# Kernel tuning notes

Hardware: AMD Instinct MI355X
Metric: run time of the kernel (lower is better)

The kernel has to match this reference:

```python
import jax, jax.numpy as jnp
import numpy as np

N, E, IN, HID, OUT = 50000, 800000, 128, 96, 2


def setup_inputs() -> dict:
    key = jax.random.key(0)
    ks = jax.random.split(key, 10)
    x = jax.random.normal(ks[0], (N, IN), jnp.float32)
    edge_index = jax.random.randint(ks[1], (2, E), 0, N, dtype=jnp.int64)
    # PQVA mask: per-node, first output channel is a "known" quantity (masked out),
    # second is the prediction target -> ~mask selects exactly N elements.
    m = np.zeros((N, OUT), dtype=bool)
    m[:, 0] = True
    PQVA_mask = jnp.asarray(m)
    scaler_mean = 0.1 * jax.random.normal(ks[2], (IN,), jnp.float32)
    scaler_std = 0.5 + jax.random.uniform(ks[3], (IN,), jnp.float32)  # in [0.5, 1.5)
    W1 = jax.random.normal(ks[4], (IN, HID), jnp.float32) / np.sqrt(IN)
    W2 = jax.random.normal(ks[5], (HID, HID), jnp.float32) / np.sqrt(HID)
    W3 = jax.random.normal(ks[6], (HID, HID), jnp.float32) / np.sqrt(HID)
    Wout = jax.random.normal(ks[7], (HID, OUT), jnp.float32) / np.sqrt(HID)
    b1 = jnp.zeros((HID,), jnp.float32)
    b2 = jnp.zeros((HID,), jnp.float32)
    b3 = jnp.zeros((HID,), jnp.float32)
    bout = jnp.zeros((OUT,), jnp.float32)
    return {"x": x, "edge_index": edge_index, "PQVA_mask": PQVA_mask,
            "scaler_mean": scaler_mean, "scaler_std": scaler_std,
            "W1": W1, "b1": b1, "W2": W2, "b2": b2, "W3": W3, "b3": b3,
            "Wout": Wout, "bout": bout}


def reference(x, edge_index, PQVA_mask, scaler_mean, scaler_std,
              W1, b1, W2, b2, W3, b3, Wout, bout):
    n = x.shape[0]
    loop = jnp.arange(n, dtype=edge_index.dtype)
    src = jnp.concatenate([edge_index[0], loop])  # add self-loops (GCNConv default)
    dst = jnp.concatenate([edge_index[1], loop])
    deg = jax.ops.segment_sum(jnp.ones_like(dst, x.dtype), dst, num_segments=n)
    dinv = jax.lax.rsqrt(deg)  # deg >= 1 thanks to self-loops
    norm = (dinv[src] * dinv[dst])[:, None]  # [E+N, 1]

    def prop(h):  # D^-1/2 (A+I) D^-1/2 @ h  via gather-scale-scatter
        return jax.ops.segment_sum(h[src] * norm, dst, num_segments=n)

    h = (x - scaler_mean) / scaler_std          # standard scaler
    h = jax.nn.relu(prop(h @ W1) + b1)          # GCNConv 1 + ReLU
    h = jax.nn.relu(prop(h @ W2) + b2)          # GCNConv 2 + ReLU
    h = prop(h @ W3) + b3                       # GCNConv 3 (last, no act)
    out = h @ Wout + bout                       # final Linear -> [N, OUT]
    # masked reshape: ~mask has exactly one True per node -> [N]
    return out.reshape(-1)[~PQVA_mask.reshape(-1)]
```

## Files before the change

### kernel.cpp

```cpp
#include <hip/hip_runtime.h>
#include <hip/hip_fp16.h>

#define IN_F 128
#define HID_F 96
#define PB 512
#define STRIDE 6144
#define MAXB 8192

typedef _Float16 f16x8 __attribute__((ext_vector_type(8)));
typedef float f32x4 __attribute__((ext_vector_type(4)));

__device__ __forceinline__ void swizzle_one(const float* W, __half* Wsw, int idx) {
    int j  = idx & 7;
    int ln = (idx >> 3) & 63;
    int ct = idx >> 9;
    int t = ct % 6, c = ct / 6;
    int k   = c * 32 + (ln >> 4) * 8 + j;
    int col = t * 16 + (ln & 15);
    Wsw[idx] = (__half)W[k * 96 + col];
}


__global__ __launch_bounds__(256) void part_prep_kernel(
        const int* __restrict__ srcv, const int* __restrict__ dstv,
        int* __restrict__ bcur, int* __restrict__ ebuf, int E,
        const float* __restrict__ stdv, float* __restrict__ rstd,
        const float* __restrict__ W3, const float* __restrict__ Wout,
        const float* __restrict__ b3, const float* __restrict__ bout,
        float* __restrict__ wv, float* __restrict__ cconst,
        const float* __restrict__ W1, __half* __restrict__ Wsw1, int SW1,
        const float* __restrict__ W2, __half* __restrict__ Wsw2, int SW2) {
    int b = blockIdx.x, t = threadIdx.x;
    if (b >= PB) {
        int pb = b - PB;
        if (pb == 0) {
            if (t < IN_F) rstd[t] = 1.0f / stdv[t];
            if (t < HID_F) {
                float s = 0.f;
                for (int j = 0; j < HID_F; ++j) s += W3[t * HID_F + j] * Wout[j * 2 + 1];
                wv[t] = s;
            }
            if (t == 0) {
                float s = 0.f;
                for (int j = 0; j < HID_F; ++j) s += b3[j] * Wout[j * 2 + 1];
                cconst[0] = s + bout[1];
            }
        } else if (pb <= 48) {
            int idx = (pb - 1) * 256 + t;
            if (idx < SW1) swizzle_one(W1, Wsw1, idx);
        } else {
            int idx = (pb - 49) * 256 + t;
            if (idx < SW2) swizzle_one(W2, Wsw2, idx);
        }
        return;
    }
    __shared__ int h[256];
    __shared__ int cur[256];
    int chunk = (E + PB - 1) / PB;
    int s = b * chunk;
    int eend = min(s + chunk, E);
    h[t] = 0;
    __syncthreads();
    for (int e = s + t; e < eend; e += 256) atomicAdd(&h[dstv[e] >> 8], 1);
    __syncthreads();
    if (h[t]) cur[t] = t * STRIDE + atomicAdd(&bcur[t], h[t]);
    __syncthreads();
    for (int e = s + t; e < eend; e += 256) {
        int sv = srcv[e], d = dstv[e];
        int p = atomicAdd(&cur[d >> 8], 1);
        ebuf[p] = (sv << 8) | (d & 255);
    }
}


__global__ __launch_bounds__(256) void buildcsr_kernel(
        const int* __restrict__ ebuf, const int* __restrict__ bcur,
        int* __restrict__ rowdeg, float* __restrict__ dinv,
        int* __restrict__ cols, int n) {
    __shared__ int dg[256];
    __shared__ int tmp[256];
    __shared__ int cur[256];
    __shared__ int colst[MAXB];
    int t = threadIdx.x;
    int k = blockIdx.x;
    int seg = k * STRIDE;
    int cnt = min(bcur[k], STRIDE);
    dg[t] = 0;
    __syncthreads();
    for (int i = t; i < cnt; i += 256) atomicAdd(&dg[ebuf[seg + i] & 255], 1);
    __syncthreads();
    int v = dg[t];
    tmp[t] = v;
    __syncthreads();
#pragma unroll
    for (int off = 1; off < 256; off <<= 1) {
        int u = (t >= off) ? tmp[t - off] : 0;
        __syncthreads();
        tmp[t] += u;
        __syncthreads();
    }
    int excl = tmp[t] - v;
    int node = (k << 8) + t;
    if (node < n) {
        rowdeg[node] = ((seg + excl) << 9) | v;
        dinv[node] = rsqrtf((float)v + 1.0f);
    }
    cur[t] = excl;
    __syncthreads();
    for (int i = t; i < cnt; i += 256) {
        int p = ebuf[seg + i];
        int lp = atomicAdd(&cur[p & 255], 1);
        colst[lp] = ((unsigned)p) >> 8;
    }
    __syncthreads();
    for (int i = t; i < cnt; i += 256) cols[seg + i] = colst[i];
}


template<int MODE, int K>
__global__ __launch_bounds__(256) void gemm_mfma_kernel(
        const void* __restrict__ Ain, const __half* __restrict__ Wsw,
        const float* __restrict__ mean, const float* __restrict__ rstd,
        const float* __restrict__ dinv, __half* __restrict__ C, int n) {
    constexpr int NCH = K / 32;
    int lane = threadIdx.x & 63;
    int wv_  = threadIdx.x >> 6;
    int m = lane & 15, q = lane >> 4;
    int node0 = blockIdx.x * 64 + wv_ * 16;
    int g = node0 + m;
    int gc = g < n ? g : n - 1;

    f32x4 acc[6];
#pragma unroll
    for (int t = 0; t < 6; ++t) acc[t] = (f32x4){0.f, 0.f, 0.f, 0.f};

#pragma unroll
    for (int c = 0; c < NCH; ++c) {
        f16x8 a;
        if (MODE == 0) {
            const float* ap = (const float*)Ain + (long)gc * K + c * 32 + q * 8;
            float4 v0 = *(const float4*)ap;
            float4 v1 = *(const float4*)(ap + 4);
            float4 m0 = *(const float4*)(mean + c * 32 + q * 8);
            float4 m1 = *(const float4*)(mean + c * 32 + q * 8 + 4);
            float4 r0 = *(const float4*)(rstd + c * 32 + q * 8);
            float4 r1 = *(const float4*)(rstd + c * 32 + q * 8 + 4);
            a[0] = (_Float16)((v0.x - m0.x) * r0.x);
            a[1] = (_Float16)((v0.y - m0.y) * r0.y);
            a[2] = (_Float16)((v0.z - m0.z) * r0.z);
            a[3] = (_Float16)((v0.w - m0.w) * r0.w);
            a[4] = (_Float16)((v1.x - m1.x) * r1.x);
            a[5] = (_Float16)((v1.y - m1.y) * r1.y);
            a[6] = (_Float16)((v1.z - m1.z) * r1.z);
            a[7] = (_Float16)((v1.w - m1.w) * r1.w);
        } else {
            a = *(const f16x8*)((const __half*)Ain + (long)gc * K + c * 32 + q * 8);
        }
#pragma unroll
        for (int t = 0; t < 6; ++t) {
            f16x8 b = *(const f16x8*)(Wsw + (size_t)(((c * 6) + t) * 64 + lane) * 8);
            acc[t] = __builtin_amdgcn_mfma_f32_16x16x32_f16(a, b, acc[t], 0, 0, 0);
        }
    }
    float dv[4];
#pragma unroll
    for (int r = 0; r < 4; ++r) {
        int gr = node0 + q * 4 + r;
        dv[r] = (gr < n) ? dinv[gr] : 0.f;
    }
#pragma unroll
    for (int t = 0; t < 6; ++t)
#pragma unroll
        for (int r = 0; r < 4; ++r) {
            int gr = node0 + q * 4 + r;
            if (gr < n) C[(long)gr * 96 + t * 16 + m] = (__half)(acc[t][r] * dv[r]);
        }
}


template<int DOT>
__global__ __launch_bounds__(256) void prop16_kernel(
        const __half* __restrict__ hin, const int* __restrict__ rowdeg,
        const int* __restrict__ cols,
        const float* __restrict__ dinv, const float* __restrict__ bias,
        const float* __restrict__ wvv, __half* __restrict__ hout,
        float* __restrict__ zs, int n) {
    int wid = (blockIdx.x * blockDim.x + threadIdx.x) >> 6;
    int lane = threadIdx.x & 63;
    if (wid >= n) return;
    int rd = rowdeg[wid];
    int e0 = ((unsigned)rd) >> 9;
    int e1 = e0 + (rd & 511);
    bool active = lane < 48;
    int g = lane / 12, l = lane - g * 12;
    int gg = active ? g : 0;
    const f16x8* hp = (const f16x8*)hin;

    float acc[8];
#pragma unroll
    for (int j = 0; j < 8; ++j) acc[j] = 0.f;

    int e = e0;
    for (; e + 16 <= e1; e += 16) {
        int c0 = cols[e + gg];
        int c1 = cols[e + 4 + gg];
        int c2 = cols[e + 8 + gg];
        int c3 = cols[e + 12 + gg];
        f16x8 v0 = hp[(long)c0 * 12 + l];
        f16x8 v1 = hp[(long)c1 * 12 + l];
        f16x8 v2 = hp[(long)c2 * 12 + l];
        f16x8 v3 = hp[(long)c3 * 12 + l];
#pragma unroll
        for (int j = 0; j < 8; ++j)
            acc[j] += (float)v0[j] + (float)v1[j] + (float)v2[j] + (float)v3[j];
    }
    for (; e <= e1; e += 4) {
        int idx = e + gg;
        bool isedge = idx < e1;
        int c = wid;
        if (isedge) c = cols[idx];
        f16x8 v = hp[(long)c * 12 + l];
        float fm = (active && idx <= e1) ? 1.f : 0.f;
#pragma unroll
        for (int j = 0; j < 8; ++j) acc[j] += fm * (float)v[j];
    }
#pragma unroll
    for (int j = 0; j < 8; ++j) {
        acc[j] += __shfl_down(acc[j], 24, 64);
        acc[j] += __shfl_down(acc[j], 12, 64);
    }
    float di = dinv[wid];
    if (DOT == 0) {
        if (lane < 12) {
            float4 b0 = *(const float4*)(bias + lane * 8);
            float4 b1 = *(const float4*)(bias + lane * 8 + 4);
            f16x8 o;
            o[0] = (_Float16)fmaxf(di * acc[0] + b0.x, 0.f);
            o[1] = (_Float16)fmaxf(di * acc[1] + b0.y, 0.f);
            o[2] = (_Float16)fmaxf(di * acc[2] + b0.z, 0.f);
            o[3] = (_Float16)fmaxf(di * acc[3] + b0.w, 0.f);
            o[4] = (_Float16)fmaxf(di * acc[4] + b1.x, 0.f);
            o[5] = (_Float16)fmaxf(di * acc[5] + b1.y, 0.f);
            o[6] = (_Float16)fmaxf(di * acc[6] + b1.z, 0.f);
            o[7] = (_Float16)fmaxf(di * acc[7] + b1.w, 0.f);
            *(f16x8*)(hout + (long)wid * 96 + lane * 8) = o;
        }
    } else {
        float v = 0.f;
        if (lane < 12) {
            float4 b0 = *(const float4*)(bias + lane * 8);
            float4 b1 = *(const float4*)(bias + lane * 8 + 4);
            float4 w0 = *(const float4*)(wvv + lane * 8);
            float4 w1 = *(const float4*)(wvv + lane * 8 + 4);
            v  = fmaxf(di * acc[0] + b0.x, 0.f) * w0.x;
            v += fmaxf(di * acc[1] + b0.y, 0.f) * w0.y;
            v += fmaxf(di * acc[2] + b0.z, 0.f) * w0.z;
            v += fmaxf(di * acc[3] + b0.w, 0.f) * w0.w;
            v += fmaxf(di * acc[4] + b1.x, 0.f) * w1.x;
            v += fmaxf(di * acc[5] + b1.y, 0.f) * w1.y;
            v += fmaxf(di * acc[6] + b1.z, 0.f) * w1.z;
            v += fmaxf(di * acc[7] + b1.w, 0.f) * w1.w;
        }
#pragma unroll
        for (int off = 32; off; off >>= 1) v += __shfl_xor(v, off, 64);
        if (lane == 0) zs[wid] = di * v;
    }
}


__global__ __launch_bounds__(256) void prop_scalar_kernel(
        const float* __restrict__ zs, const int* __restrict__ rowdeg,
        const int* __restrict__ cols,
        const float* __restrict__ dinv, const float* __restrict__ cconst,
        float* __restrict__ out, int n) {
    int i = blockIdx.x * blockDim.x + threadIdx.x;
    if (i >= n) return;
    int rd = rowdeg[i];
    int e0 = ((unsigned)rd) >> 9;
    int e1 = e0 + (rd & 511);
    float s = 0.f;
    int e = e0;
    for (; e + 4 <= e1; e += 4) {
        int c0 = cols[e + 0], c1 = cols[e + 1], c2 = cols[e + 2], c3 = cols[e + 3];
        s += zs[c0]; s += zs[c1]; s += zs[c2]; s += zs[c3];
    }
    for (; e < e1; ++e) s += zs[cols[e]];
    out[i] = dinv[i] * (s + zs[i]) + cconst[0];
}


extern "C" void kernel_launch(void* const* d_in, const int* in_sizes, int n_in,
                              void* d_out, int out_size, void* d_ws, size_t ws_size,
                              hipStream_t stream) {
    const float* x    = (const float*)d_in[0];
    const int*   eidx = (const int*)d_in[1];
    const float* mean = (const float*)d_in[3];
    const float* stdv = (const float*)d_in[4];
    const float* W1   = (const float*)d_in[5];
    const float* b1   = (const float*)d_in[6];
    const float* W2   = (const float*)d_in[7];
    const float* b2   = (const float*)d_in[8];
    const float* W3   = (const float*)d_in[9];
    const float* b3   = (const float*)d_in[10];
    const float* Wout = (const float*)d_in[11];
    const float* bout = (const float*)d_in[12];
    float* out = (float*)d_out;

    const int n = in_sizes[0] / IN_F;
    const int E = in_sizes[1] / 2;
    const int* srcv = eidx;
    const int* dstv = eidx + E;
    const int NB = (n + 255) >> 8;

    char* ws = (char*)d_ws;
    size_t off = 0;
    auto alloc = [&](size_t bytes) -> void* {
        void* p = ws + off;
        off = (off + bytes + 255) & ~(size_t)255;
        return p;
    };
    const int SW1 = 4 * 6 * 64 * 8;
    const int SW2 = 3 * 6 * 64 * 8;
    int*    rowdeg = (int*)alloc((size_t)n * 4);
    float*  dinv   = (float*)alloc((size_t)n * 4);
    int*    cols   = (int*)alloc((size_t)256 * STRIDE * 4);
    int*    ebuf   = (int*)alloc((size_t)256 * STRIDE * 4);
    int*    bcur   = (int*)alloc(256 * 4);
    float*  rstd   = (float*)alloc(IN_F * 4);
    float*  wv     = (float*)alloc(HID_F * 4);
    float*  cconst = (float*)alloc(4);
    float*  zbuf   = (float*)alloc((size_t)n * 4);
    __half* Wsw1   = (__half*)alloc((size_t)SW1 * 2);
    __half* Wsw2   = (__half*)alloc((size_t)SW2 * 2);
    __half* bufA   = (__half*)alloc((size_t)n * HID_F * 2);
    __half* bufB   = (__half*)alloc((size_t)n * HID_F * 2);

    hipMemsetAsync(bcur, 0, 256 * 4, stream);

    part_prep_kernel<<<PB + 85, 256, 0, stream>>>(
        srcv, dstv, bcur, ebuf, E,
        stdv, rstd, W3, Wout, b3, bout, wv, cconst,
        W1, Wsw1, SW1, W2, Wsw2, SW2);
    buildcsr_kernel<<<NB, 256, 0, stream>>>(ebuf, bcur, rowdeg, dinv, cols, n);

    int gemm_grid = (n + 63) / 64;
    int prop_grid = (int)(((long)n * 64 + 255) / 256);

    gemm_mfma_kernel<0, IN_F><<<gemm_grid, 256, 0, stream>>>(x, Wsw1, mean, rstd, dinv,
                                                             bufA, n);
    prop16_kernel<0><<<prop_grid, 256, 0, stream>>>(bufA, rowdeg, cols, dinv, b1,
                                                    nullptr, bufB, nullptr, n);
    gemm_mfma_kernel<1, HID_F><<<gemm_grid, 256, 0, stream>>>(bufB, Wsw2, nullptr, nullptr,
                                                              dinv, bufA, n);
    prop16_kernel<1><<<prop_grid, 256, 0, stream>>>(bufA, rowdeg, cols, dinv, b2,
                                                    wv, nullptr, zbuf, n);
    prop_scalar_kernel<<<(n + 255) / 256, 256, 0, stream>>>(zbuf, rowdeg, cols, dinv,
                                                            cconst, out, n);
}
```

Before: 210.6 us.

## Fuse first GEMM into partition kernel and apply source scaling in propagation

Moves the first-layer GEMM (scaler plus W1 multiply) into the edge-partition kernel as extra blocks, with W1 swizzled into LDS per block. This removes a separate launch and lets the GEMM overlap with edge bucketing. Because dinv is not yet known at that point, the first propagation now multiplies each gathered neighbour by dinv[src]. That adds an extra random gather per edge, and each block re-swizzles W1 redundantly.

```diff
diff --git a/kernel.cpp b/kernel.cpp
--- a/kernel.cpp
+++ b/kernel.cpp
@@ -21,54 +21,107 @@
 }
 
 
-__global__ __launch_bounds__(256) void part_prep_kernel(
+__global__ __launch_bounds__(256) void mega_a_kernel(
         const int* __restrict__ srcv, const int* __restrict__ dstv,
         int* __restrict__ bcur, int* __restrict__ ebuf, int E,
-        const float* __restrict__ stdv, float* __restrict__ rstd,
+        const float* __restrict__ x, const float* __restrict__ mean,
+        const float* __restrict__ stdv, __half* __restrict__ bufA, int n, int g1,
+        const float* __restrict__ W1,
+        const float* __restrict__ W2, __half* __restrict__ Wsw2, int SW2,
         const float* __restrict__ W3, const float* __restrict__ Wout,
         const float* __restrict__ b3, const float* __restrict__ bout,
-        float* __restrict__ wv, float* __restrict__ cconst,
-        const float* __restrict__ W1, __half* __restrict__ Wsw1, int SW1,
-        const float* __restrict__ W2, __half* __restrict__ Wsw2, int SW2) {
+        float* __restrict__ wv, float* __restrict__ cconst) {
+    __shared__ __align__(16) int smem[6144];
     int b = blockIdx.x, t = threadIdx.x;
-    if (b >= PB) {
-        int pb = b - PB;
-        if (pb == 0) {
-            if (t < IN_F) rstd[t] = 1.0f / stdv[t];
-            if (t < HID_F) {
-                float s = 0.f;
-                for (int j = 0; j < HID_F; ++j) s += W3[t * HID_F + j] * Wout[j * 2 + 1];
-                wv[t] = s;
+
+    if (b < PB) {
+        int* h = smem;
+        int* cur = smem + 256;
+        int chunk = (E + PB - 1) / PB;
+        int s = b * chunk;
+        int eend = min(s + chunk, E);
+        h[t] = 0;
+        __syncthreads();
+        for (int e = s + t; e < eend; e += 256) atomicAdd(&h[dstv[e] >> 8], 1);
+        __syncthreads();
+        if (h[t]) cur[t] = t * STRIDE + atomicAdd(&bcur[t], h[t]);
+        __syncthreads();
+        for (int e = s + t; e < eend; e += 256) {
+            int sv = srcv[e], d = dstv[e];
+            int p = atomicAdd(&cur[d >> 8], 1);
+            ebuf[p] = (sv << 8) | (d & 255);
+        }
+        return;
+    }
+    if (b < PB + g1) {
+        __half* wlds = (__half*)smem;
+        for (int idx = t; idx < 12288; idx += 256) {
+            int j  = idx & 7;
+            int ln = (idx >> 3) & 63;
+            int ct = idx >> 9;
+            int tt = ct % 6, c = ct / 6;
+            int k   = c * 32 + (ln >> 4) * 8 + j;
+            int col = tt * 16 + (ln & 15);
+            wlds[idx] = (__half)W1[k * 96 + col];
+        }
+        __syncthreads();
+        int lane = t & 63;
+        int wv_  = t >> 6;
+        int m = lane & 15, q = lane >> 4;
+        int node0 = (b - PB) * 64 + wv_ * 16;
+        int g = node0 + m;
+        int gc = g < n ? g : n - 1;
+        f32x4 acc[6];
+#pragma unroll
+        for (int tt = 0; tt < 6; ++tt) acc[tt] = (f32x4){0.f, 0.f, 0.f, 0.f};
+#pragma unroll
+        for (int c = 0; c < 4; ++c) {
+            const float* ap = x + (long)gc * IN_F + c * 32 + q * 8;
+            float4 v0 = *(const float4*)ap;
+            float4 v1 = *(const float4*)(ap + 4);
+            float4 m0 = *(const float4*)(mean + c * 32 + q * 8);
+            float4 m1 = *(const float4*)(mean + c * 32 + q * 8 + 4);
+            float4 s0 = *(const float4*)(stdv + c * 32 + q * 8);
+            float4 s1 = *(const float4*)(stdv + c * 32 + q * 8 + 4);
+            f16x8 a;
+            a[0] = (_Float16)((v0.x - m0.x) / s0.x);
+            a[1] = (_Float16)((v0.y - m0.y) / s0.y);
+            a[2] = (_Float16)((v0.z - m0.z) / s0.z);
+            a[3] = (_Float16)((v0.w - m0.w) / s0.w);
+            a[4] = (_Float16)((v1.x - m1.x) / s1.x);
+            a[5] = (_Float16)((v1.y - m1.y) / s1.y);
+            a[6] = (_Float16)((v1.z - m1.z) / s1.z);
+            a[7] = (_Float16)((v1.w - m1.w) / s1.w);
+#pragma unroll
+            for (int tt = 0; tt < 6; ++tt) {
+                f16x8 bf = *(const f16x8*)(wlds + (size_t)(((c * 6) + tt) * 64 + lane) * 8);
+                acc[tt] = __builtin_amdgcn_mfma_f32_16x16x32_f16(a, bf, acc[tt], 0, 0, 0);
             }
-            if (t == 0) {
-                float s = 0.f;
-                for (int j = 0; j < HID_F; ++j) s += b3[j] * Wout[j * 2 + 1];
-                cconst[0] = s + bout[1];
+        }
+#pragma unroll
+        for (int tt = 0; tt < 6; ++tt)
+#pragma unroll
+            for (int r = 0; r < 4; ++r) {
+                int gr = node0 + q * 4 + r;
+                if (gr < n) bufA[(long)gr * 96 + tt * 16 + m] = (__half)acc[tt][r];
             }
-        } else if (pb <= 48) {
-            int idx = (pb - 1) * 256 + t;
-            if (idx < SW1) swizzle_one(W1, Wsw1, idx);
-        } else {
-            int idx = (pb - 49) * 256 + t;
-            if (idx < SW2) swizzle_one(W2, Wsw2, idx);
-        }
         return;
     }
-    __shared__ int h[256];
-    __shared__ int cur[256];
-    int chunk = (E + PB - 1) / PB;
-    int s = b * chunk;
-    int eend = min(s + chunk, E);
-    h[t] = 0;
-    __syncthreads();
-    for (int e = s + t; e < eend; e += 256) atomicAdd(&h[dstv[e] >> 8], 1);
-    __syncthreads();
-    if (h[t]) cur[t] = t * STRIDE + atomicAdd(&bcur[t], h[t]);
-    __syncthreads();
-    for (int e = s + t; e < eend; e += 256) {
-        int sv = srcv[e], d = dstv[e];
-        int p = atomicAdd(&cur[d >> 8], 1);
-        ebuf[p] = (sv << 8) | (d & 255);
+    int pb = b - PB - g1;
+    if (pb < 36) {
+        int idx = pb * 256 + t;
+        if (idx < SW2) swizzle_one(W2, Wsw2, idx);
+        return;
+    }
+    if (t < HID_F) {
+        float s = 0.f;
+        for (int j = 0; j < HID_F; ++j) s += W3[t * HID_F + j] * Wout[j * 2 + 1];
+        wv[t] = s;
+    }
+    if (t == 0) {
+        float s = 0.f;
+        for (int j = 0; j < HID_F; ++j) s += b3[j] * Wout[j * 2 + 1];
+        cconst[0] = s + bout[1];
     }
 }
 
@@ -117,12 +170,9 @@
 }
 
 
-template<int MODE, int K>
-__global__ __launch_bounds__(256) void gemm_mfma_kernel(
-        const void* __restrict__ Ain, const __half* __restrict__ Wsw,
-        const float* __restrict__ mean, const float* __restrict__ rstd,
+__global__ __launch_bounds__(256) void gemm2_kernel(
+        const __half* __restrict__ Ain, const __half* __restrict__ Wsw,
         const float* __restrict__ dinv, __half* __restrict__ C, int n) {
-    constexpr int NCH = K / 32;
     int lane = threadIdx.x & 63;
     int wv_  = threadIdx.x >> 6;
     int m = lane & 15, q = lane >> 4;
@@ -133,29 +183,9 @@
     f32x4 acc[6];
 #pragma unroll
     for (int t = 0; t < 6; ++t) acc[t] = (f32x4){0.f, 0.f, 0.f, 0.f};
-
-#pragma unroll
-    for (int c = 0; c < NCH; ++c) {
-        f16x8 a;
-        if (MODE == 0) {
-            const float* ap = (const float*)Ain + (long)gc * K + c * 32 + q * 8;
-            float4 v0 = *(const float4*)ap;
-            float4 v1 = *(const float4*)(ap + 4);
-            float4 m0 = *(const float4*)(mean + c * 32 + q * 8);
-            float4 m1 = *(const float4*)(mean + c * 32 + q * 8 + 4);
-            float4 r0 = *(const float4*)(rstd + c * 32 + q * 8);
-            float4 r1 = *(const float4*)(rstd + c * 32 + q * 8 + 4);
-            a[0] = (_Float16)((v0.x - m0.x) * r0.x);
-            a[1] = (_Float16)((v0.y - m0.y) * r0.y);
-            a[2] = (_Float16)((v0.z - m0.z) * r0.z);
-            a[3] = (_Float16)((v0.w - m0.w) * r0.w);
-            a[4] = (_Float16)((v1.x - m1.x) * r1.x);
-            a[5] = (_Float16)((v1.y - m1.y) * r1.y);
-            a[6] = (_Float16)((v1.z - m1.z) * r1.z);
-            a[7] = (_Float16)((v1.w - m1.w) * r1.w);
-        } else {
-            a = *(const f16x8*)((const __half*)Ain + (long)gc * K + c * 32 + q * 8);
-        }
+#pragma unroll
+    for (int c = 0; c < 3; ++c) {
+        f16x8 a = *(const f16x8*)(Ain + (long)gc * HID_F + c * 32 + q * 8);
 #pragma unroll
         for (int t = 0; t < 6; ++t) {
             f16x8 b = *(const f16x8*)(Wsw + (size_t)(((c * 6) + t) * 64 + lane) * 8);
@@ -178,7 +208,7 @@
 }
 
 
-template<int DOT>
+template<int DOT, int ESC>
 __global__ __launch_bounds__(256) void prop16_kernel(
         const __half* __restrict__ hin, const int* __restrict__ rowdeg,
         const int* __restrict__ cols,
@@ -206,13 +236,16 @@
         int c1 = cols[e + 4 + gg];
         int c2 = cols[e + 8 + gg];
         int c3 = cols[e + 12 + gg];
+        float w0 = 1.f, w1 = 1.f, w2 = 1.f, w3 = 1.f;
+        if (ESC) { w0 = dinv[c0]; w1 = dinv[c1]; w2 = dinv[c2]; w3 = dinv[c3]; }
         f16x8 v0 = hp[(long)c0 * 12 + l];
         f16x8 v1 = hp[(long)c1 * 12 + l];
         f16x8 v2 = hp[(long)c2 * 12 + l];
         f16x8 v3 = hp[(long)c3 * 12 + l];
 #pragma unroll
         for (int j = 0; j < 8; ++j)
-            acc[j] += (float)v0[j] + (float)v1[j] + (float)v2[j] + (float)v3[j];
+            acc[j] += w0 * (float)v0[j] + w1 * (float)v1[j]
+                    + w2 * (float)v2[j] + w3 * (float)v3[j];
     }
     for (; e <= e1; e += 4) {
         int idx = e + gg;
@@ -220,9 +253,9 @@
         int c = wid;
         if (isedge) c = cols[idx];
         f16x8 v = hp[(long)c * 12 + l];
-        float fm = (active && idx <= e1) ? 1.f : 0.f;
-#pragma unroll
-        for (int j = 0; j < 8; ++j) acc[j] += fm * (float)v[j];
+        float w = (active && idx <= e1) ? (ESC ? dinv[c] : 1.f) : 0.f;
+#pragma unroll
+        for (int j = 0; j < 8; ++j) acc[j] += w * (float)v[j];
     }
 #pragma unroll
     for (int j = 0; j < 8; ++j) {
@@ -319,41 +352,37 @@
         off = (off + bytes + 255) & ~(size_t)255;
         return p;
     };
-    const int SW1 = 4 * 6 * 64 * 8;
     const int SW2 = 3 * 6 * 64 * 8;
     int*    rowdeg = (int*)alloc((size_t)n * 4);
     float*  dinv   = (float*)alloc((size_t)n * 4);
     int*    cols   = (int*)alloc((size_t)256 * STRIDE * 4);
     int*    ebuf   = (int*)alloc((size_t)256 * STRIDE * 4);
     int*    bcur   = (int*)alloc(256 * 4);
-    float*  rstd   = (float*)alloc(IN_F * 4);
     float*  wv     = (float*)alloc(HID_F * 4);
     float*  cconst = (float*)alloc(4);
     float*  zbuf   = (float*)alloc((size_t)n * 4);
-    __half* Wsw1   = (__half*)alloc((size_t)SW1 * 2);
     __half* Wsw2   = (__half*)alloc((size_t)SW2 * 2);
     __half* bufA   = (__half*)alloc((size_t)n * HID_F * 2);
     __half* bufB   = (__half*)alloc((size_t)n * HID_F * 2);
 
     hipMemsetAsync(bcur, 0, 256 * 4, stream);
 
-    part_prep_kernel<<<PB + 85, 256, 0, stream>>>(
+    int g1 = (n + 63) / 64;
+
+    mega_a_kernel<<<PB + g1 + 37, 256, 0, stream>>>(
         srcv, dstv, bcur, ebuf, E,
-        stdv, rstd, W3, Wout, b3, bout, wv, cconst,
-        W1, Wsw1, SW1, W2, Wsw2, SW2);
+        x, mean, stdv, bufA, n, g1,
+        W1, W2, Wsw2, SW2, W3, Wout, b3, bout, wv, cconst);
+
     buildcsr_kernel<<<NB, 256, 0, stream>>>(ebuf, bcur, rowdeg, dinv, cols, n);
 
-    int gemm_grid = (n + 63) / 64;
     int prop_grid = (int)(((long)n * 64 + 255) / 256);
 
-    gemm_mfma_kernel<0, IN_F><<<gemm_grid, 256, 0, stream>>>(x, Wsw1, mean, rstd, dinv,
-                                                             bufA, n);
-    prop16_kernel<0><<<prop_grid, 256, 0, stream>>>(bufA, rowdeg, cols, dinv, b1,
-                                                    nullptr, bufB, nullptr, n);
-    gemm_mfma_kernel<1, HID_F><<<gemm_grid, 256, 0, stream>>>(bufB, Wsw2, nullptr, nullptr,
-                                                              dinv, bufA, n);
-    prop16_kernel<1><<<prop_grid, 256, 0, stream>>>(bufA, rowdeg, cols, dinv, b2,
-                                                    wv, nullptr, zbuf, n);
+    prop16_kernel<0, 1><<<prop_grid, 256, 0, stream>>>(bufA, rowdeg, cols, dinv, b1,
+                                                       nullptr, bufB, nullptr, n);
+    gemm2_kernel<<<g1, 256, 0, stream>>>(bufB, Wsw2, dinv, bufA, n);
+    prop16_kernel<1, 0><<<prop_grid, 256, 0, stream>>>(bufA, rowdeg, cols, dinv, b2,
+                                                       wv, nullptr, zbuf, n);
     prop_scalar_kernel<<<(n + 255) / 256, 256, 0, stream>>>(zbuf, rowdeg, cols, dinv,
                                                             cconst, out, n);
 }
```

New measurement: 216.4 us. +2.8%, slower.
